# Kernel optimization log

Measured on AMD Instinct MI355X. Metric: run time of the kernel, lower is better.

The kernel has to match this reference:

```python
import jax, jax.numpy as jnp
import numpy as np

B, N, M, D = 32, 1024, 1024, 256


def setup_inputs() -> dict:
    key = jax.random.key(0)
    k1, k2, k3, k4 = jax.random.split(key, 4)
    h1 = jax.random.normal(k1, (B, N, D), dtype=jnp.float32)
    h2 = jax.random.normal(k2, (B, M, D), dtype=jnp.float32)
    W = jax.random.normal(k3, (D,), dtype=jnp.float32) * (1.0 / np.sqrt(D))
    b = jax.random.normal(k4, (1,), dtype=jnp.float32) * (1.0 / np.sqrt(D))
    return {"h1": h1, "h2": h2, "W": W, "b": b}


def reference(h1, h2, W, b):
    # Pairwise squared L2 distance (p=2, abs(x-y)^2 == (x-y)^2), halved as in the
    # original: dist_matrix = cdist(g1, g2) / 2.0. Use the ||x||^2+||y||^2-2xy
    # expansion to avoid materializing the [B,N,M,D] difference tensor.
    sq1 = jnp.sum(h1 * h1, axis=-1)                      # [B, N]
    sq2 = jnp.sum(h2 * h2, axis=-1)                      # [B, M]
    cross = jnp.einsum('bnd,bmd->bnm', h1, h2)           # [B, N, M]
    dist = jnp.maximum(sq1[:, :, None] + sq2[:, None, :] - 2.0 * cross, 0.0) * 0.5

    # Insertion/deletion cost: |Linear(h)| per node.
    d1 = jnp.abs(jnp.einsum('bnd,d->bn', h1, W) + b)     # [B, N]
    d2 = jnp.abs(jnp.einsum('bmd,d->bm', h2, W) + b)     # [B, M]

    a = jnp.minimum(jnp.min(dist, axis=1), d2)           # min over rows -> [B, M]
    bb = jnp.minimum(jnp.min(dist, axis=2), d1)          # min over cols -> [B, N]
    d = jnp.mean(a, axis=-1) + jnp.mean(bb, axis=-1)     # [B]
    return d
```

## Files before the change

### kernel.cpp

```cpp
#include <hip/hip_runtime.h>


#define B_  32
#define N_  1024
#define D_  256
#define BN_ (B_ * N_)
#define TILE 128
#define BK   32

typedef short bf16x8 __attribute__((ext_vector_type(8)));
typedef float f32x4  __attribute__((ext_vector_type(4)));
typedef unsigned short u16;
typedef unsigned int   u32;

__device__ __forceinline__ u16 f2bf(float x) {
  u32 u = __float_as_uint(x);
  u += 0x7fffu + ((u >> 16) & 1u);
  return (u16)(u >> 16);
}

__device__ __forceinline__ void gload16(const void* g, void* l) {
  __builtin_amdgcn_global_load_lds((const __attribute__((address_space(1))) u32*)g,
                                   (__attribute__((address_space(3))) u32*)l, 16, 0, 0);
}


__global__ __launch_bounds__(256) void prep_kernel(
    const float* __restrict__ h1, const float* __restrict__ h2,
    const float* __restrict__ W, const float* __restrict__ bias,
    u16* __restrict__ bfA, u16* __restrict__ bfB, int strideSh,
    float* __restrict__ fl) {
  const int tid = threadIdx.x, lane = tid & 63, wid = tid >> 6;
  const int gw  = blockIdx.x * 4 + wid;
  const int isB = gw >> 15;
  const int row = gw & 32767;

  const float4 v = *(const float4*)((isB ? h2 : h1) + (size_t)row * D_ + lane * 4);
  const float4 w = *(const float4*)(W + lane * 4);
  float sq = v.x * v.x + v.y * v.y + v.z * v.z + v.w * v.w;
  float dw = v.x * w.x + v.y * w.y + v.z * w.z + v.w * w.w;
#pragma unroll
  for (int off = 1; off < 64; off <<= 1) {
    sq += __shfl_xor(sq, off);
    dw += __shfl_xor(dw, off);
  }

  const ushort4 o = {f2bf(v.x), f2bf(v.y), f2bf(v.z), f2bf(v.w)};
  *(ushort4*)((isB ? bfB : bfA) + (size_t)row * strideSh + lane * 4) = o;

  if (lane == 0) {
    fl[isB * BN_ + row]       = fabsf(dw + bias[0]);
    fl[(2 + isB) * BN_ + row] = sq;
  }
  if (lane == 1) ((u32*)fl)[(4 + isB) * BN_ + row] = 0x7f7f7f7fu;
}

__global__ __launch_bounds__(256) void gemm_kernel(
    const u16* __restrict__ bfA, const u16* __restrict__ bfB, int strideSh,
    float* __restrict__ fl) {
  __shared__ __align__(16) u16 As[TILE * BK];
  __shared__ __align__(16) u16 Bs[TILE * BK];
  __shared__ float sqrow[TILE], sqcol[TILE];
  __shared__ float rowred[TILE][2], colred[TILE][2];

  const int bid = blockIdx.x;
  const int b   = ((bid >> 9) << 3) + (bid & 7);
  const int t6  = (bid >> 3) & 63;
  const int bm  = t6 & 7;
  const int bn  = t6 >> 3;

  const int tid = threadIdx.x, lane = tid & 63, wid = tid >> 6;
  const int wr = wid >> 1, wc = wid & 1;

  if (tid < TILE) sqrow[tid] = fl[2 * BN_ + b * N_ + bn * TILE + tid];
  else            sqcol[tid - TILE] = fl[3 * BN_ + b * N_ + bm * TILE + (tid - TILE)];

  const char* srcA[2]; const char* srcB[2];
#pragma unroll
  for (int c = 0; c < 2; ++c) {
    const int o   = (wid * 2 + c) * 1024 + lane * 16;
    const int lin = o ^ (((o >> 6) & 7) << 4);
    const int row = lin >> 6;
    const int kb  = lin & 63;
    srcA[c] = (const char*)(bfA + (size_t)(b * N_ + bn * TILE + row) * strideSh) + kb;
    srcB[c] = (const char*)(bfB + (size_t)(b * N_ + bm * TILE + row) * strideSh) + kb;
  }

  f32x4 acc[4][4];
#pragma unroll
  for (int i = 0; i < 4; ++i)
#pragma unroll
    for (int j = 0; j < 4; ++j) acc[i][j] = (f32x4){0.f, 0.f, 0.f, 0.f};

  const int arow = wr * 64 + (lane & 15);
  const int brow = wc * 64 + (lane & 15);
  const int aoff = (arow * 64 + ((lane >> 4) * 16)) ^ ((arow & 7) << 4);
  const int boff = (brow * 64 + ((lane >> 4) * 16)) ^ ((brow & 7) << 4);
  const char* ab = (const char*)As;
  const char* bb = (const char*)Bs;

#pragma unroll 1
  for (int ks = 0; ks < 8; ++ks) {
#pragma unroll
    for (int c = 0; c < 2; ++c) {
      gload16(srcA[c], &As[(wid * 2 + c) * 512]);
      gload16(srcB[c], &Bs[(wid * 2 + c) * 512]);
      srcA[c] += 64; srcB[c] += 64;
    }
    __syncthreads();
    bf16x8 af[4], bfv[4];
#pragma unroll
    for (int mi = 0; mi < 4; ++mi) af[mi]  = *(const bf16x8*)(ab + aoff + mi * 1024);
#pragma unroll
    for (int nj = 0; nj < 4; ++nj) bfv[nj] = *(const bf16x8*)(bb + boff + nj * 1024);
#pragma unroll
    for (int mi = 0; mi < 4; ++mi)
#pragma unroll
      for (int nj = 0; nj < 4; ++nj)
        acc[mi][nj] = __builtin_amdgcn_mfma_f32_16x16x32_bf16(af[mi], bfv[nj], acc[mi][nj], 0, 0, 0);
    __syncthreads();
  }

  float sj[4];
#pragma unroll
  for (int nj = 0; nj < 4; ++nj) sj[nj] = sqcol[wc * 64 + nj * 16 + (lane & 15)];

  float rminv[4][4];
  float cminv[4] = {3.0e38f, 3.0e38f, 3.0e38f, 3.0e38f};
#pragma unroll
  for (int mi = 0; mi < 4; ++mi)
#pragma unroll
    for (int r = 0; r < 4; ++r) {
      const float si = sqrow[wr * 64 + mi * 16 + (lane >> 4) * 4 + r];
      float rm = 3.0e38f;
#pragma unroll
      for (int nj = 0; nj < 4; ++nj) {
        const float dd = fmaxf(fmaf(-2.f, acc[mi][nj][r], si + sj[nj]), 0.f) * 0.5f;
        rm = fminf(rm, dd);
        cminv[nj] = fminf(cminv[nj], dd);
      }
      rminv[mi][r] = rm;
    }

#pragma unroll
  for (int mi = 0; mi < 4; ++mi)
#pragma unroll
    for (int r = 0; r < 4; ++r) {
      float v = rminv[mi][r];
      v = fminf(v, __shfl_xor(v, 1));
      v = fminf(v, __shfl_xor(v, 2));
      v = fminf(v, __shfl_xor(v, 4));
      v = fminf(v, __shfl_xor(v, 8));
      rminv[mi][r] = v;
    }
  if ((lane & 15) == 0) {
#pragma unroll
    for (int mi = 0; mi < 4; ++mi)
#pragma unroll
      for (int r = 0; r < 4; ++r)
        rowred[wr * 64 + mi * 16 + (lane >> 4) * 4 + r][wc] = rminv[mi][r];
  }

#pragma unroll
  for (int nj = 0; nj < 4; ++nj) {
    float v = cminv[nj];
    v = fminf(v, __shfl_xor(v, 16));
    v = fminf(v, __shfl_xor(v, 32));
    cminv[nj] = v;
  }
  if (lane < 16) {
#pragma unroll
    for (int nj = 0; nj < 4; ++nj)
      colred[wc * 64 + nj * 16 + lane][wr] = cminv[nj];
  }
  __syncthreads();

  u32* rming = (u32*)(fl + 4 * BN_);
  u32* cming = (u32*)(fl + 5 * BN_);
  if (tid < TILE) {
    const float v = fminf(rowred[tid][0], rowred[tid][1]);
    atomicMin(&rming[b * N_ + bn * TILE + tid], __float_as_uint(v));
  } else {
    const int c = tid - TILE;
    const float v = fminf(colred[c][0], colred[c][1]);
    atomicMin(&cming[b * N_ + bm * TILE + c], __float_as_uint(v));
  }
}

__global__ __launch_bounds__(256) void finish_kernel(
    const float* __restrict__ fl, float* __restrict__ out) {
  const int b = blockIdx.x;
  const int tid = threadIdx.x;
  const float* dd1  = fl + b * N_;
  const float* dd2  = fl + BN_ + b * N_;
  const float* rmin = fl + 4 * BN_ + b * N_;
  const float* cmin = fl + 5 * BN_ + b * N_;

  float s = 0.f;
  for (int i = tid; i < N_; i += 256)
    s += fminf(rmin[i], dd1[i]) + fminf(cmin[i], dd2[i]);

  __shared__ float sm[4];
  for (int off = 32; off; off >>= 1) s += __shfl_down(s, off);
  if ((tid & 63) == 0) sm[tid >> 6] = s;
  __syncthreads();
  if (tid == 0) out[b] = (sm[0] + sm[1] + sm[2] + sm[3]) * (1.f / 1024.f);
}

extern "C" void kernel_launch(void* const* d_in, const int* in_sizes, int n_in,
                              void* d_out, int out_size, void* d_ws, size_t ws_size,
                              hipStream_t stream) {
  (void)in_sizes; (void)n_in; (void)out_size;
  const float* h1   = (const float*)d_in[0];
  const float* h2   = (const float*)d_in[1];
  const float* W    = (const float*)d_in[2];
  const float* bias = (const float*)d_in[3];
  float* out = (float*)d_out;

  const size_t BF_BYTES = (size_t)BN_ * D_ * 2;
  const size_t NEED     = 2 * BF_BYTES + 6u * BN_ * 4;

  u16 *bfA, *bfB; int strideSh; float* fl;
  if (ws_size >= NEED) {
    bfA = (u16*)d_ws;
    bfB = (u16*)((char*)d_ws + BF_BYTES);
    strideSh = D_;
    fl = (float*)((char*)d_ws + 2 * BF_BYTES);
  } else {
    bfA = (u16*)d_in[0];
    bfB = (u16*)d_in[1];
    strideSh = 2 * D_;
    fl = (float*)d_ws;
  }

  prep_kernel<<<dim3(16384), 256, 0, stream>>>(h1, h2, W, bias, bfA, bfB, strideSh, fl);
  gemm_kernel<<<dim3(2048), 256, 0, stream>>>(bfA, bfB, strideSh, fl);
  finish_kernel<<<dim3(B_), 256, 0, stream>>>(fl, out);
}
```

Before: 144.5 us.

## Double-buffer GEMM LDS tiles and remap prep blocks per XCD

The GEMM main loop now uses two LDS buffers, so the global-to-LDS load for the next K step is issued before computing on the current one, with one barrier per iteration instead of two. This is meant to hide global load latency behind the MFMA work. The prep kernel's block-to-row mapping is also changed so each XCD processes whole batches, aiming to keep the bf16 data the GEMM later reads for that batch in the same XCD's L2. LDS use doubles, which may lower occupancy.

```diff
diff --git a/kernel.cpp b/kernel.cpp
--- a/kernel.cpp
+++ b/kernel.cpp
@@ -31,9 +31,14 @@
     u16* __restrict__ bfA, u16* __restrict__ bfB, int strideSh,
     float* __restrict__ fl) {
   const int tid = threadIdx.x, lane = tid & 63, wid = tid >> 6;
-  const int gw  = blockIdx.x * 4 + wid;
-  const int isB = gw >> 15;
-  const int row = gw & 32767;
+  const int bid = blockIdx.x;
+  const int xcd = bid & 7;
+  const int i   = bid >> 3;
+  const int g   = (i >> 9) * 8 + xcd;
+  const int r9  = i & 511;
+  const int rows4 = r9 * 4 + wid;
+  const int isB = rows4 >> 10;
+  const int row = g * N_ + (rows4 & 1023);
 
   const float4 v = *(const float4*)((isB ? h2 : h1) + (size_t)row * D_ + lane * 4);
   const float4 w = *(const float4*)(W + lane * 4);
@@ -58,8 +63,8 @@
 __global__ __launch_bounds__(256) void gemm_kernel(
     const u16* __restrict__ bfA, const u16* __restrict__ bfB, int strideSh,
     float* __restrict__ fl) {
-  __shared__ __align__(16) u16 As[TILE * BK];
-  __shared__ __align__(16) u16 Bs[TILE * BK];
+  __shared__ __align__(16) u16 As[2][TILE * BK];
+  __shared__ __align__(16) u16 Bs[2][TILE * BK];
   __shared__ float sqrow[TILE], sqcol[TILE];
   __shared__ float rowred[TILE][2], colred[TILE][2];
 
@@ -96,18 +101,18 @@
   const int brow = wc * 64 + (lane & 15);
   const int aoff = (arow * 64 + ((lane >> 4) * 16)) ^ ((arow & 7) << 4);
   const int boff = (brow * 64 + ((lane >> 4) * 16)) ^ ((brow & 7) << 4);
-  const char* ab = (const char*)As;
-  const char* bb = (const char*)Bs;
-
-#pragma unroll 1
-  for (int ks = 0; ks < 8; ++ks) {
-#pragma unroll
-    for (int c = 0; c < 2; ++c) {
-      gload16(srcA[c], &As[(wid * 2 + c) * 512]);
-      gload16(srcB[c], &Bs[(wid * 2 + c) * 512]);
-      srcA[c] += 64; srcB[c] += 64;
+
+  auto stage = [&](int c) {
+#pragma unroll
+    for (int q = 0; q < 2; ++q) {
+      gload16(srcA[q], &As[c][(wid * 2 + q) * 512]);
+      gload16(srcB[q], &Bs[c][(wid * 2 + q) * 512]);
+      srcA[q] += 64; srcB[q] += 64;
     }
-    __syncthreads();
+  };
+  auto compute = [&](int c) {
+    const char* ab = (const char*)As[c];
+    const char* bb = (const char*)Bs[c];
     bf16x8 af[4], bfv[4];
 #pragma unroll
     for (int mi = 0; mi < 4; ++mi) af[mi]  = *(const bf16x8*)(ab + aoff + mi * 1024);
@@ -118,8 +123,19 @@
 #pragma unroll
       for (int nj = 0; nj < 4; ++nj)
         acc[mi][nj] = __builtin_amdgcn_mfma_f32_16x16x32_bf16(af[mi], bfv[nj], acc[mi][nj], 0, 0, 0);
+  };
+
+  stage(0);
+  __syncthreads();
+  int cur = 0;
+#pragma unroll 1
+  for (int ks = 0; ks < 7; ++ks) {
+    stage(cur ^ 1);
+    compute(cur);
     __syncthreads();
-  }
+    cur ^= 1;
+  }
+  compute(cur);
 
   float sj[4];
 #pragma unroll
```

New measurement: 146.3 us. About the same (+1.3%).
